# Kernel optimization log

Hardware: AMD Instinct MI355X
Metric: run time of the kernel (lower is better)

The kernel has to match this reference:

```python
import jax, jax.numpy as jnp
import numpy as np
from jax.scipy.special import logsumexp

T, B, V, U = 1000, 32, 1000, 100
BLANK = 0
NEG_EPS = float(np.log(1e-30))  # original code uses log(0 + 1e-30) as 'zero' init
NEG_INF = float('-inf')


def setup_inputs() -> dict:
    key = jax.random.key(0)
    k1, k2, k3, k4 = jax.random.split(key, 4)
    return {
        "log_probs": jax.random.normal(k1, (T, B, V), jnp.float32),
        "targets": jax.random.randint(k2, (B, U), 1, V),            # labels in [1, V), blank=0 excluded
        "input_lengths": jax.random.randint(k3, (B,), T // 2, T + 1),
        "target_lengths": jax.random.randint(k4, (B,), U // 2, U + 1),
    }


def _ctc_losses(log_probs, targets, input_lengths, target_lengths):
    Tm, Bm, _ = log_probs.shape
    Um = targets.shape[1]
    S = 2 * Um + 1
    # module re-applies log_softmax over the class dim
    x = jax.nn.log_softmax(log_probs, axis=-1)  # [T,B,V]

    s = jnp.arange(S)
    lab = jnp.take(targets, jnp.clip(s // 2, 0, Um - 1), axis=1)   # [B,S]
    z = jnp.where((s % 2 == 0)[None, :], BLANK, lab)               # extended label seq [B,S]
    z_m2 = jnp.concatenate([jnp.full((Bm, 2), -1, z.dtype), z[:, :-2]], axis=1)
    # skip transition allowed iff s>=2, z[s]!=blank, z[s]!=z[s-2]
    allow_skip = (z != BLANK) & (z != z_m2) & (s >= 2)[None, :]    # [B,S]

    e0 = jnp.take_along_axis(x[0], z, axis=1)                      # [B,S]
    alpha0 = jnp.full((Bm, S), NEG_EPS, x.dtype)
    alpha0 = alpha0.at[:, 0].set(x[0, :, BLANK])
    alpha0 = alpha0.at[:, 1].set(e0[:, 1])

    neg_col = jnp.full((Bm, 1), NEG_INF, x.dtype)

    def step(alpha, inp):
        x_t, t = inp
        e = jnp.take_along_axis(x_t, z, axis=1)                    # emissions [B,S]
        a1 = jnp.concatenate([neg_col, alpha[:, :-1]], axis=1)     # alpha[s-1]
        a2 = jnp.concatenate([neg_col, neg_col, alpha[:, :-2]], axis=1)
        a2 = jnp.where(allow_skip, a2, NEG_INF)                    # alpha[s-2] if skip allowed
        new = logsumexp(jnp.stack([alpha, a1, a2]), axis=0) + e
        # freeze alpha past each example's input length
        alpha = jnp.where((t < input_lengths)[:, None], new, alpha)
        return alpha, None

    ts = jnp.arange(1, Tm)
    alpha_f, _ = jax.lax.scan(step, alpha0, (x[1:], ts))
    # loss_i = -logsumexp(alpha[T_i-1, S_i-2:S_i]) with S_i = 2*u_i+1
    idx = jnp.stack([2 * target_lengths - 1, 2 * target_lengths], axis=1)  # [B,2]
    last2 = jnp.take_along_axis(alpha_f, idx, axis=1)
    return -logsumexp(last2, axis=1)  # reduction='none' (default)


def reference(log_probs, targets, input_lengths, target_lengths):
    return _ctc_losses(log_probs, targets, input_lengths, target_lengths)
```

## Files before the change

### kernel.cpp

```cpp
#include <hip/hip_runtime.h>
#include <math.h>

#define TDIM 1000
#define BDIM 32
#define VDIM 1000
#define UDIM 100
#define SDIM 201
#define EROW 104
#define LN2   0.6931471805599453f
#define PIPE 16
#define SCALE_EXP 110

typedef __attribute__((ext_vector_type(2))) float f32x2;
typedef __attribute__((ext_vector_type(4))) int   i32x4;

__device__ __forceinline__ float med3c(float x) {
    return __builtin_amdgcn_fmed3f(x, 0.f, 1.f);
}

template <int CTRL>
__device__ __forceinline__ float dppadd(float v) {
    int r = __builtin_amdgcn_update_dpp(
        0, __builtin_bit_cast(int, v), CTRL, 0xf, 0xf, true);
    return v + __builtin_bit_cast(float, r);
}

__global__ __launch_bounds__(256) void k_lsm_gather(
    const float* __restrict__ lp, const int* __restrict__ targets,
    const int* __restrict__ tlen, float* __restrict__ etab)
{
    const int w = threadIdx.x >> 6, l = threadIdx.x & 63;
    const int row = blockIdx.x * 4 + w;
    const int t = row / BDIM;
    const int b = row - t * BDIM;
    const float* base = lp + (size_t)row * VDIM;
    const float4* p4 = (const float4*)base;

    float4 v0 = p4[l];
    float4 v1 = p4[64 + l];
    float4 v2 = p4[128 + l];
    float4 v3;
    if (l < 58) v3 = p4[192 + l];
    else        v3 = make_float4(-INFINITY, -INFINITY, -INFINITY, -INFINITY);

    float s = __expf(v0.x) + __expf(v0.y) + __expf(v0.z) + __expf(v0.w)
            + __expf(v1.x) + __expf(v1.y) + __expf(v1.z) + __expf(v1.w)
            + __expf(v2.x) + __expf(v2.y) + __expf(v2.z) + __expf(v2.w)
            + __expf(v3.x) + __expf(v3.y) + __expf(v3.z) + __expf(v3.w);
    s = dppadd<0xB1>(s);
    s = dppadd<0x4E>(s);
    s = dppadd<0x141>(s);
    s = dppadd<0x140>(s);
    s += __shfl_xor(s, 16);
    s += __shfl_xor(s, 32);

    const float inv_s = __builtin_amdgcn_rcpf(s);
    float* erow = etab + (size_t)(b * TDIM + t) * EROW;
    const int Sb = 2 * tlen[b];
    if (l < 50) {
        const int c0 = targets[b * UDIM + 2 * l];
        const int c1 = targets[b * UDIM + 2 * l + 1];
        const float mk1 = (4 * l + 1 <= Sb) ? 1.f : 0.f;
        const float mk3 = (4 * l + 3 <= Sb) ? 1.f : 0.f;
        float2 o;
        o.x = med3c(__expf(base[c0]) * inv_s) * mk1;
        o.y = med3c(__expf(base[c1]) * inv_s) * mk3;
        *(float2*)(erow + 2 * l) = o;
    } else if (l == 50) {
        float2 o;
        o.x = med3c(__expf(base[0]) * inv_s);
        o.y = 0.f;
        *(float2*)(erow + 100) = o;
    }
}

__device__ __forceinline__ float dpp_shr1_zero(float x) {
    int r = __builtin_amdgcn_update_dpp(
        0, __builtin_bit_cast(int, x), 0x138, 0xf, 0xf, true);
    return __builtin_bit_cast(float, r);
}

template <int CTRL>
__device__ __forceinline__ float dppmax(float v) {
    int r = __builtin_amdgcn_update_dpp(
        0, __builtin_bit_cast(int, v), CTRL, 0xf, 0xf, true);
    return fmaxf(v, __builtin_bit_cast(float, r));
}

__global__ __launch_bounds__(64, 1) void k_alpha(
    const float* __restrict__ etab, const int* __restrict__ targets,
    const int* __restrict__ ilen, const int* __restrict__ tlen,
    float* __restrict__ out)
{
    const int b = blockIdx.x;
    const int l = threadIdx.x;
    const float* eb = etab + (size_t)b * TDIM * EROW;
    const int eoff = (2 * l <= 100) ? 2 * l : 100;
    const float* plane = eb + eoff;

    f32x2 g = {0.f, 0.f};
    if (l < 50) {
        const int c0 = targets[b * UDIM + 2 * l];
        const int c1 = targets[b * UDIM + 2 * l + 1];
        g.y = (c1 != c0) ? 1.f : 0.f;
        if (l >= 1) g.x = (c0 != targets[b * UDIM + 2 * l - 1]) ? 1.f : 0.f;
    }

    const int u_b = tlen[b];
    const int Sb  = 2 * u_b;

    f32x2 pr0 = *(const f32x2*)plane;
    const float bl0 = __builtin_bit_cast(float,
        __builtin_amdgcn_readlane(__builtin_bit_cast(int, pr0.x), 50));
    const float F = 1e-30f * 0x1p110f;
    f32x2 E, O;
    E.x = (4 * l     <= Sb) ? F : 0.f;
    E.y = (4 * l + 2 <= Sb) ? F : 0.f;
    O.x = (4 * l + 1 <= Sb) ? F : 0.f;
    O.y = (4 * l + 3 <= Sb) ? F : 0.f;
    if (l == 0) {
        E.x = bl0   * 0x1p110f;
        O.x = pr0.x * 0x1p110f;
    }
    int ksum = -SCALE_EXP;

    int L = ilen[b];
    if (L > TDIM) L = TDIM;

    const unsigned long long ebu = (unsigned long long)eb;
    i32x4 srd;
    srd.x = (int)(ebu & 0xffffffffu);
    srd.y = (int)((ebu >> 32) & 0xffffu);
    srd.z = TDIM * EROW * 4;
    srd.w = 0x00020000;
    const int voff = eoff * 4;
    int so = EROW * 4;

#define STEP(LAB_) {                                                             \
    const float ebv = __builtin_bit_cast(float,                                  \
        __builtin_amdgcn_readlane(__builtin_bit_cast(int, (LAB_).x), 50));       \
    f32x2 ebp; ebp.x = ebv; ebp.y = ebv;                                         \
    const float pP3 = dpp_shr1_zero(O.y);                                        \
    f32x2 sk; sk.x = pP3; sk.y = O.x;                                            \
    const f32x2 T  = E + O;                                                      \
    const f32x2 ev = (E + sk) * ebp;                                             \
    const f32x2 od = (sk * g + T) * (LAB_);                                      \
    E = ev; O = od; }

#define RESCALE() {                                                              \
    float pm = fmaxf(__builtin_amdgcn_fmed3f(                                    \
        fmaxf(E.x, O.x), fmaxf(E.y, O.y), INFINITY), 0x1p-10f);                  \
    pm = dppmax<0xB1>(pm);                                  \
    pm = dppmax<0x4E>(pm);                                  \
    pm = dppmax<0x141>(pm);                                 \
    pm = dppmax<0x140>(pm);                                 \
    pm = dppmax<0x142>(pm);                                  \
    pm = dppmax<0x143>(pm);                                  \
    const int mb = __builtin_amdgcn_readlane(__builtin_bit_cast(int, pm), 63);   \
    const int ex = (mb >> 23) & 0xff;                                            \
    ksum += ex - (127 + SCALE_EXP);                                              \
    const float sc = __builtin_bit_cast(float, ((254 + SCALE_EXP) - ex) << 23);  \
    f32x2 scv; scv.x = sc; scv.y = sc;                                           \
    E = E * scv; O = O * scv; }

#define ISS(J, OFFP)                                                             \
    asm volatile("buffer_load_dwordx2 %0, %1, %2, %3 offen offset:" OFFP         \
        : "=v"(lab[J]) : "v"(voff), "s"(srd), "s"(so));

#define ISS8(G) \
    ISS((G)+0, "0");    ISS((G)+1, "416");                                       \
    ISS((G)+2, "832");  ISS((G)+3, "1248");                                      \
    ISS((G)+4, "1664"); ISS((G)+5, "2080");                                      \
    ISS((G)+6, "2496"); ISS((G)+7, "2912");

#define WAITG8(J) asm volatile("s_waitcnt vmcnt(8)"                              \
    : "+v"(lab[(J)]),   "+v"(lab[(J)+1]), "+v"(lab[(J)+2]), "+v"(lab[(J)+3]),    \
      "+v"(lab[(J)+4]), "+v"(lab[(J)+5]), "+v"(lab[(J)+6]), "+v"(lab[(J)+7]));

#define GROUP8(G) {                                                              \
    WAITG8(G);                                                                   \
    STEP(lab[(G)+0]); STEP(lab[(G)+1]);                                          \
    STEP(lab[(G)+2]); STEP(lab[(G)+3]);                                          \
    STEP(lab[(G)+4]); STEP(lab[(G)+5]);                                          \
    STEP(lab[(G)+6]); STEP(lab[(G)+7]);                                          \
    ISS8(G);                                                                     \
    so += 3328;                                                                  \
    RESCALE(); }

    f32x2 lab[PIPE];
    ISS8(0);  so += 3328;
    ISS8(8);  so += 3328;

    int t = 1;
    for (; t + PIPE - 1 < L; t += PIPE) {
        GROUP8(0);
        GROUP8(8);
    }
    asm volatile("s_waitcnt vmcnt(0)" ::: "memory");

    for (; t < L; ++t) {
        f32x2 lb = *(const f32x2*)(plane + (size_t)t * EROW);
        STEP(lb);
        RESCALE();
    }
#undef GROUP8
#undef WAITG8
#undef ISS8
#undef ISS
#undef RESCALE
#undef STEP

    __shared__ float A[256];
    A[4 * l + 0] = __builtin_amdgcn_logf(fmaxf(E.x, 1e-38f));
    A[4 * l + 1] = __builtin_amdgcn_logf(fmaxf(O.x, 1e-38f));
    A[4 * l + 2] = __builtin_amdgcn_logf(fmaxf(E.y, 1e-38f));
    A[4 * l + 3] = __builtin_amdgcn_logf(fmaxf(O.y, 1e-38f));
    __syncthreads();
    if (l == 0) {
        const float x1 = A[2 * u_b - 1], x2 = A[2 * u_b];
        const float mx = fmaxf(x1, x2), mn = fminf(x1, x2);
        const float lse2 = mx + __builtin_amdgcn_logf(
            1.f + __builtin_amdgcn_exp2f(mn - mx));
        out[b] = -(LN2 * (lse2 + (float)ksum));
    }
}

extern "C" void kernel_launch(void* const* d_in, const int* in_sizes, int n_in,
                              void* d_out, int out_size, void* d_ws, size_t ws_size,
                              hipStream_t stream) {
    const float* lp      = (const float*)d_in[0];
    const int*   targets = (const int*)d_in[1];
    const int*   ilen    = (const int*)d_in[2];
    const int*   tlen    = (const int*)d_in[3];
    float* out  = (float*)d_out;
    float* etab = (float*)d_ws;

    k_lsm_gather<<<TDIM * BDIM / 4, 256, 0, stream>>>(lp, targets, tlen, etab);
    k_alpha<<<BDIM, 64, 0, stream>>>(etab, targets, ilen, tlen, out);
}
```

Before: 69.84 us.

## Make softmax-gather kernel persistent with double-buffered raw buffer loads

Swaps the one-row-per-wave grid for a persistent grid of 2048 blocks. Each wave walks rows with a stride and double-buffers the row loads using inline-asm buffer_load_dwordx4 and explicit vmcnt waits. The next row's 4KB load overlaps the current row's exp/reduce/gather work, and launch and block-scheduling overhead drops. The risk is lower occupancy-driven latency hiding and fragile asm waitcnt handling. The fourth load reads past row end for lanes 58+, but those values are masked, and only the last row can touch the buffer range limit.

```diff
diff --git a/kernel.cpp b/kernel.cpp
--- a/kernel.cpp
+++ b/kernel.cpp
@@ -9,9 +9,13 @@
 #define EROW 104
 #define LN2   0.6931471805599453f
 #define PIPE 16
+#define NROWS (TDIM * BDIM)
+#define P1_BLOCKS 2048
+#define P1_STRIDE (P1_BLOCKS * 4)
 #define SCALE_EXP 110
 
 typedef __attribute__((ext_vector_type(2))) float f32x2;
+typedef __attribute__((ext_vector_type(4))) float f32x4;
 typedef __attribute__((ext_vector_type(4))) int   i32x4;
 
 __device__ __forceinline__ float med3c(float x) {
@@ -25,66 +29,118 @@
     return v + __builtin_bit_cast(float, r);
 }
 
+__device__ __forceinline__ float dpp_shr1_zero(float x) {
+    int r = __builtin_amdgcn_update_dpp(
+        0, __builtin_bit_cast(int, x), 0x138, 0xf, 0xf, true);
+    return __builtin_bit_cast(float, r);
+}
+
+template <int CTRL>
+__device__ __forceinline__ float dppmax(float v) {
+    int r = __builtin_amdgcn_update_dpp(
+        0, __builtin_bit_cast(int, v), CTRL, 0xf, 0xf, true);
+    return fmaxf(v, __builtin_bit_cast(float, r));
+}
+
 __global__ __launch_bounds__(256) void k_lsm_gather(
     const float* __restrict__ lp, const int* __restrict__ targets,
     const int* __restrict__ tlen, float* __restrict__ etab)
 {
     const int w = threadIdx.x >> 6, l = threadIdx.x & 63;
-    const int row = blockIdx.x * 4 + w;
-    const int t = row / BDIM;
-    const int b = row - t * BDIM;
-    const float* base = lp + (size_t)row * VDIM;
-    const float4* p4 = (const float4*)base;
-
-    float4 v0 = p4[l];
-    float4 v1 = p4[64 + l];
-    float4 v2 = p4[128 + l];
-    float4 v3;
-    if (l < 58) v3 = p4[192 + l];
-    else        v3 = make_float4(-INFINITY, -INFINITY, -INFINITY, -INFINITY);
-
-    float s = __expf(v0.x) + __expf(v0.y) + __expf(v0.z) + __expf(v0.w)
-            + __expf(v1.x) + __expf(v1.y) + __expf(v1.z) + __expf(v1.w)
-            + __expf(v2.x) + __expf(v2.y) + __expf(v2.z) + __expf(v2.w)
-            + __expf(v3.x) + __expf(v3.y) + __expf(v3.z) + __expf(v3.w);
-    s = dppadd<0xB1>(s);
-    s = dppadd<0x4E>(s);
-    s = dppadd<0x141>(s);
-    s = dppadd<0x140>(s);
-    s += __shfl_xor(s, 16);
-    s += __shfl_xor(s, 32);
-
-    const float inv_s = __builtin_amdgcn_rcpf(s);
-    float* erow = etab + (size_t)(b * TDIM + t) * EROW;
-    const int Sb = 2 * tlen[b];
-    if (l < 50) {
-        const int c0 = targets[b * UDIM + 2 * l];
-        const int c1 = targets[b * UDIM + 2 * l + 1];
-        const float mk1 = (4 * l + 1 <= Sb) ? 1.f : 0.f;
-        const float mk3 = (4 * l + 3 <= Sb) ? 1.f : 0.f;
-        float2 o;
-        o.x = med3c(__expf(base[c0]) * inv_s) * mk1;
-        o.y = med3c(__expf(base[c1]) * inv_s) * mk3;
-        *(float2*)(erow + 2 * l) = o;
-    } else if (l == 50) {
-        float2 o;
-        o.x = med3c(__expf(base[0]) * inv_s);
-        o.y = 0.f;
-        *(float2*)(erow + 100) = o;
-    }
-}
-
-__device__ __forceinline__ float dpp_shr1_zero(float x) {
-    int r = __builtin_amdgcn_update_dpp(
-        0, __builtin_bit_cast(int, x), 0x138, 0xf, 0xf, true);
-    return __builtin_bit_cast(float, r);
-}
-
-template <int CTRL>
-__device__ __forceinline__ float dppmax(float v) {
-    int r = __builtin_amdgcn_update_dpp(
-        0, __builtin_bit_cast(int, v), CTRL, 0xf, 0xf, true);
-    return fmaxf(v, __builtin_bit_cast(float, r));
+    const int gw = blockIdx.x * 4 + w;
+
+    const unsigned long long lpu = (unsigned long long)lp;
+    i32x4 srd;
+    srd.x = (int)(lpu & 0xffffffffu);
+    srd.y = (int)((lpu >> 32) & 0xffffu);
+    srd.z = NROWS * VDIM * 4;
+    srd.w = 0x00020000;
+
+#define P1_ISSUE(R0_, R1_, R2_, R3_, ROW_) {                                     \
+    const int _vo = (ROW_) * (VDIM * 4) + l * 16;                                \
+    asm volatile("buffer_load_dwordx4 %0, %1, %2, 0 offen offset:0"              \
+        : "=v"(R0_) : "v"(_vo), "s"(srd));                                       \
+    asm volatile("buffer_load_dwordx4 %0, %1, %2, 0 offen offset:1024"           \
+        : "=v"(R1_) : "v"(_vo), "s"(srd));                                       \
+    asm volatile("buffer_load_dwordx4 %0, %1, %2, 0 offen offset:2048"           \
+        : "=v"(R2_) : "v"(_vo), "s"(srd));                                       \
+    asm volatile("buffer_load_dwordx4 %0, %1, %2, 0 offen offset:3072"           \
+        : "=v"(R3_) : "v"(_vo), "s"(srd)); }
+
+#define P1_WAIT4(R0_, R1_, R2_, R3_)                                             \
+    asm volatile("s_waitcnt vmcnt(4)" : "+v"(R0_), "+v"(R1_), "+v"(R2_), "+v"(R3_));
+#define P1_WAIT0(R0_, R1_, R2_, R3_)                                             \
+    asm volatile("s_waitcnt vmcnt(0)" : "+v"(R0_), "+v"(R1_), "+v"(R2_), "+v"(R3_));
+
+#define P1_BODY(V0_, V1_, V2_, V3_, ROW_) {                                      \
+    f32x4 v3m = (V3_);                                                           \
+    if (l >= 58) { v3m.x = -INFINITY; v3m.y = -INFINITY;                         \
+                   v3m.z = -INFINITY; v3m.w = -INFINITY; }                       \
+    float s = __expf((V0_).x) + __expf((V0_).y) + __expf((V0_).z) + __expf((V0_).w) \
+            + __expf((V1_).x) + __expf((V1_).y) + __expf((V1_).z) + __expf((V1_).w) \
+            + __expf((V2_).x) + __expf((V2_).y) + __expf((V2_).z) + __expf((V2_).w) \
+            + __expf(v3m.x) + __expf(v3m.y) + __expf(v3m.z) + __expf(v3m.w);     \
+    s = dppadd<0xB1>(s);                                    \
+    s = dppadd<0x4E>(s);                                    \
+    s = dppadd<0x141>(s);                                   \
+    s = dppadd<0x140>(s);                                   \
+    s += __shfl_xor(s, 16);                                                      \
+    s += __shfl_xor(s, 32);                                                      \
+    const float inv_s = __builtin_amdgcn_rcpf(s);                                \
+    const int _b = (ROW_) & (BDIM - 1);                                          \
+    const int _t = (ROW_) >> 5;                                                  \
+    const float* base = lp + (size_t)(ROW_) * VDIM;                              \
+    float* erow = etab + (size_t)(_b * TDIM + _t) * EROW;                        \
+    const int Sb = 2 * tlen[_b];                                                 \
+    if (l < 50) {                                                                \
+        const int c0 = targets[_b * UDIM + 2 * l];                               \
+        const int c1 = targets[_b * UDIM + 2 * l + 1];                           \
+        const float mk1 = (4 * l + 1 <= Sb) ? 1.f : 0.f;                         \
+        const float mk3 = (4 * l + 3 <= Sb) ? 1.f : 0.f;                         \
+        float2 o;                                                                \
+        o.x = med3c(__expf(base[c0]) * inv_s) * mk1;                             \
+        o.y = med3c(__expf(base[c1]) * inv_s) * mk3;                             \
+        *(float2*)(erow + 2 * l) = o;                                            \
+    } else if (l == 50) {                                                        \
+        float2 o;                                                                \
+        o.x = med3c(__expf(base[0]) * inv_s);                                    \
+        o.y = 0.f;                                                               \
+        *(float2*)(erow + 100) = o;                                              \
+    } }
+
+    f32x4 a0, a1, a2, a3;
+    f32x4 b0, b1, b2, b3;
+
+    int row = gw;
+    P1_ISSUE(a0, a1, a2, a3, row);
+    for (;;) {
+        int nxt = row + P1_STRIDE;
+        if (nxt < NROWS) {
+            P1_ISSUE(b0, b1, b2, b3, nxt);
+            P1_WAIT4(a0, a1, a2, a3);
+            P1_BODY(a0, a1, a2, a3, row);
+        } else {
+            P1_WAIT0(a0, a1, a2, a3);
+            P1_BODY(a0, a1, a2, a3, row);
+            break;
+        }
+        row = nxt;
+        nxt = row + P1_STRIDE;
+        if (nxt < NROWS) {
+            P1_ISSUE(a0, a1, a2, a3, nxt);
+            P1_WAIT4(b0, b1, b2, b3);
+            P1_BODY(b0, b1, b2, b3, row);
+        } else {
+            P1_WAIT0(b0, b1, b2, b3);
+            P1_BODY(b0, b1, b2, b3, row);
+            break;
+        }
+        row = nxt;
+    }
+#undef P1_BODY
+#undef P1_WAIT0
+#undef P1_WAIT4
+#undef P1_ISSUE
 }
 
 __global__ __launch_bounds__(64, 1) void k_alpha(
@@ -235,6 +291,6 @@
     float* out  = (float*)d_out;
     float* etab = (float*)d_ws;
 
-    k_lsm_gather<<<TDIM * BDIM / 4, 256, 0, stream>>>(lp, targets, tlen, etab);
+    k_lsm_gather<<<P1_BLOCKS, 256, 0, stream>>>(lp, targets, tlen, etab);
     k_alpha<<<BDIM, 64, 0, stream>>>(etab, targets, ilen, tlen, out);
 }
```

Measured after the change: 72.92 us. 1.04x slower.
